# Kernel tuning notes

Measured on AMD Instinct MI355X. Metric: run time of the kernel, lower is better.

The kernel has to match this reference:

```python
import jax, jax.numpy as jnp
import numpy as np

N_NODES = 50000
N_EDGES = 1600000
LORA_R = 8


def gcn_conv(h, W, b, src, dst, n):
    # PyG GCNConv: linear transform, add self-loops, symmetric normalization,
    # scatter-add aggregation at target nodes, then bias.
    h = h @ W  # [N, out]
    ones = jnp.ones(src.shape[0], dtype=h.dtype)
    deg = jax.ops.segment_sum(ones, dst, num_segments=n) + 1.0  # +1 for self-loop
    dis = jax.lax.rsqrt(deg)  # deg >= 1 always
    norm = dis[src] * dis[dst]  # [E]
    agg = jax.ops.segment_sum(norm[:, None] * h[src], dst, num_segments=n)
    agg = agg + (dis * dis)[:, None] * h  # self-loop contribution
    return agg + b


def lora(h, A, B):
    # LoRALinear: b(a(x)) * (1/r); replaces input (not additive)
    return (h @ A) @ B * (1.0 / LORA_R)


def setup_inputs() -> dict:
    key = jax.random.key(0)
    ks = jax.random.split(key, 12)
    inp = {}
    inp['x'] = jax.random.normal(ks[0], (N_NODES, 128), dtype=jnp.float32)
    inp['edge_index'] = jax.random.randint(ks[1], (2, N_EDGES), 0, N_NODES, dtype=jnp.int64 if jax.config.jax_enable_x64 else jnp.int32)
    inp['domain_idx'] = jax.random.randint(ks[2], (N_NODES,), 0, 3, dtype=jnp.int32)
    inp['emb_table'] = jax.random.normal(ks[3], (3, 4096), dtype=jnp.float32)
    s1 = 1.0 / np.sqrt(4224.0)
    inp['W1'] = jax.random.normal(ks[4], (4224, 32), dtype=jnp.float32) * s1
    inp['b1'] = jnp.zeros((32,), dtype=jnp.float32)
    inp['A1'] = jax.random.normal(ks[5], (32, LORA_R), dtype=jnp.float32) * (1.0 / np.sqrt(32.0))
    inp['B1'] = jax.random.normal(ks[6], (LORA_R, 32), dtype=jnp.float32) * (1.0 / np.sqrt(LORA_R))
    inp['W2'] = jax.random.normal(ks[7], (32, 5), dtype=jnp.float32) * (1.0 / np.sqrt(32.0))
    inp['b2'] = jnp.zeros((5,), dtype=jnp.float32)
    inp['A2'] = jax.random.normal(ks[8], (5, LORA_R), dtype=jnp.float32) * (1.0 / np.sqrt(5.0))
    inp['B2'] = jax.random.normal(ks[9], (LORA_R, 5), dtype=jnp.float32) * (1.0 / np.sqrt(LORA_R))
    return inp


def reference(x, edge_index, domain_idx, emb_table, W1, b1, A1, B1, W2, b2, A2, B2):
    n = x.shape[0]
    src, dst = edge_index[0], edge_index[1]
    embedded = emb_table[domain_idx]  # [N, 4096]
    h = jnp.concatenate([embedded, x], axis=1)  # [N, 4224]
    h = gcn_conv(h, W1, b1, src, dst, n)
    h = lora(h, A1, B1)
    h = jax.nn.relu(h)
    h = gcn_conv(h, W2, b2, src, dst, n)
    h = lora(h, A2, B2)
    return jax.nn.log_softmax(h, axis=1)
```

## Files before the change

### kernel.cpp

```cpp
#include <hip/hip_runtime.h>
#include <hip/hip_bf16.h>
#include <hip/hip_fp16.h>


#define XDIM 128
#define ODIM 5
#define EMBDIM 4096
#define TB 8192
#define BSH 6
#define BN 64
#define ECAP2 2560

__global__ void __launch_bounds__(256) k_bin(
    const int* __restrict__ src, const int* __restrict__ dst,
    unsigned int* __restrict__ sorted, int* __restrict__ bcur, int e, int ntiles,
    const float* __restrict__ emb, const float* __restrict__ W1,
    float* __restrict__ emb_part) {
    __shared__ unsigned int staged[TB];
    __shared__ int loff[1024], rctr[1024], sbase[1024];
    int t = threadIdx.x;
    if (blockIdx.x >= ntiles) {
        int bx2 = blockIdx.x - ntiles;
        int dm = bx2 >> 5, seg = bx2 & 31;
        const float* er = emb + dm * EMBDIM + seg * 128;
        const float* wr = W1 + (size_t)seg * 128 * 32;
        int j = t & 31, kk = t >> 5;
        float acc = 0.f;
        for (int k2 = kk; k2 < 128; k2 += 8) acc += er[k2] * wr[k2 * 32 + j];
        float* p = (float*)staged;
        p[kk * 32 + j] = acc;
        __syncthreads();
        if (t < 32) {
            float s = 0.f;
            #pragma unroll
            for (int r = 0; r < 8; ++r) s += p[r * 32 + t];
            emb_part[bx2 * 32 + t] = s;
        }
        return;
    }
    int base = blockIdx.x * TB;
    int len = min(TB, e - base);
    for (int i = t; i < 1024; i += 256) { loff[i] = 0; rctr[i] = 0; }
    __syncthreads();
    for (int i = t; i < len; i += 256) atomicAdd(&loff[dst[base + i] >> BSH], 1);
    __syncthreads();
    if (t < 64) {
        int ch = t * 16;
        int v[16]; int s0 = 0;
        #pragma unroll
        for (int k = 0; k < 16; ++k) { v[k] = loff[ch + k]; s0 += v[k]; }
        int pre = s0;
        #pragma unroll
        for (int d2 = 1; d2 < 64; d2 <<= 1) {
            int up = __shfl_up(pre, d2);
            if (t >= d2) pre += up;
        }
        int excl = pre - s0;
        #pragma unroll
        for (int k = 0; k < 16; ++k) { loff[ch + k] = excl; excl += v[k]; }
    }
    __syncthreads();
    for (int i = t; i < len; i += 256) {
        int s = src[base + i], d = dst[base + i];
        int b = d >> BSH;
        int r = atomicAdd(&rctr[b], 1);
        staged[loff[b] + r] = ((unsigned int)d << 16) | (unsigned int)s;
    }
    __syncthreads();
    for (int b = t; b < 1024; b += 256) {
        int l = ((b < 1023) ? loff[b + 1] : len) - loff[b];
        if (l > 0) sbase[b] = atomicAdd(&bcur[b], l);
    }
    __syncthreads();
    for (int i = t; i < len; i += 256) {
        unsigned int u = staged[i];
        int b = (int)(u >> 22);
        int pos = sbase[b] + (i - loff[b]);
        if (pos < ECAP2) sorted[(size_t)b * ECAP2 + pos] = u;
    }
}

__global__ void __launch_bounds__(256) k_disS(
    const unsigned int* __restrict__ sorted, const int* __restrict__ bcur,
    float* __restrict__ dis, int* __restrict__ deg, int n,
    const float* __restrict__ A1, const float* __restrict__ A2,
    const float* __restrict__ B2, const float* __restrict__ b1,
    const float* __restrict__ emb_part, float* __restrict__ M2,
    float* __restrict__ b1A1, float* __restrict__ emb_proj) {
    __shared__ int h[BN];
    int t = threadIdx.x, b = blockIdx.x;
    if (t < BN) h[t] = 0;
    __syncthreads();
    int m = min(bcur[b], ECAP2);
    const unsigned int* sp = sorted + (size_t)b * ECAP2;
    for (int i = t; i < m; i += 256) {
        int d = (int)(sp[i] >> 16);
        atomicAdd(&h[d & (BN - 1)], 1);
    }
    __syncthreads();
    if (t < BN) {
        int node = (b << BSH) + t;
        if (node < n) {
            deg[node] = h[t];
            dis[node] = rsqrtf((float)(h[t] + 1));
        }
    }
    if (b == 0) {
        if (t < 25) {
            int c = t / 5, cp = t % 5;
            float s = 0.f;
            #pragma unroll
            for (int r = 0; r < 8; ++r) s += A2[c * 8 + r] * B2[r * 5 + cp];
            M2[c * 5 + cp] = s * 0.125f;
        }
        if (t >= 32 && t < 40) {
            int j = t - 32;
            float s = 0.f;
            #pragma unroll
            for (int k = 0; k < 32; ++k) s += b1[k] * A1[k * 8 + j];
            b1A1[j] = s;
        }
        if (t >= 64 && t < 160) {
            int d = (t - 64) >> 5, j = (t - 64) & 31;
            float s = 0.f;
            #pragma unroll
            for (int seg = 0; seg < 32; ++seg) s += emb_part[(d * 32 + seg) * 32 + j];
            emb_proj[d * 32 + j] = s;
        }
    }
}

__global__ void __launch_bounds__(256) k_h1(const float* __restrict__ x,
                                            const int* __restrict__ dom,
                                            const float* __restrict__ emb_proj,
                                            const float* __restrict__ W1,
                                            const float* __restrict__ A1,
                                            const float* __restrict__ dis,
                                            float* __restrict__ p1s, int n) {
    __shared__ float wb[XDIM * 32];
    __shared__ float xsT[XDIM * 68];
    __shared__ float sh1[64 * 33];
    __shared__ float sA1[256];
    __shared__ int sdom[64];
    int t = threadIdx.x;
    int row0 = blockIdx.x * 64;
    {
        const float4* w4 = (const float4*)(W1 + (size_t)EMBDIM * 32);
        float4* wb4 = (float4*)wb;
        for (int i = t; i < 1024; i += 256) wb4[i] = w4[i];
    }
    sA1[t] = A1[t];
    if (t < 64) {
        int g = row0 + t;
        sdom[t] = (g < n) ? dom[g] * 32 : 0;
    }
    for (int i = t; i < 2048; i += 256) {
        int c4 = i & 31, row = i >> 5;
        int g = row0 + row;
        float4 v = (g < n) ? ((const float4*)x)[(size_t)g * 32 + c4]
                           : make_float4(0.f, 0.f, 0.f, 0.f);
        int k0 = c4 * 4;
        xsT[(k0 + 0) * 68 + row] = v.x;
        xsT[(k0 + 1) * 68 + row] = v.y;
        xsT[(k0 + 2) * 68 + row] = v.z;
        xsT[(k0 + 3) * 68 + row] = v.w;
    }
    __syncthreads();
    int rq = t >> 4, jp = t & 15;
    float a00 = 0.f, a01 = 0.f, a10 = 0.f, a11 = 0.f;
    float a20 = 0.f, a21 = 0.f, a30 = 0.f, a31 = 0.f;
    #pragma unroll 4
    for (int k = 0; k < XDIM; ++k) {
        float4 xv = *(const float4*)(xsT + k * 68 + rq * 4);
        float2 wv = *(const float2*)(wb + k * 32 + jp * 2);
        a00 += xv.x * wv.x; a01 += xv.x * wv.y;
        a10 += xv.y * wv.x; a11 += xv.y * wv.y;
        a20 += xv.z * wv.x; a21 += xv.z * wv.y;
        a30 += xv.w * wv.x; a31 += xv.w * wv.y;
    }
    int j0 = jp * 2;
    sh1[(rq * 4 + 0) * 33 + j0]     = a00 + emb_proj[sdom[rq * 4 + 0] + j0];
    sh1[(rq * 4 + 0) * 33 + j0 + 1] = a01 + emb_proj[sdom[rq * 4 + 0] + j0 + 1];
    sh1[(rq * 4 + 1) * 33 + j0]     = a10 + emb_proj[sdom[rq * 4 + 1] + j0];
    sh1[(rq * 4 + 1) * 33 + j0 + 1] = a11 + emb_proj[sdom[rq * 4 + 1] + j0 + 1];
    sh1[(rq * 4 + 2) * 33 + j0]     = a20 + emb_proj[sdom[rq * 4 + 2] + j0];
    sh1[(rq * 4 + 2) * 33 + j0 + 1] = a21 + emb_proj[sdom[rq * 4 + 2] + j0 + 1];
    sh1[(rq * 4 + 3) * 33 + j0]     = a30 + emb_proj[sdom[rq * 4 + 3] + j0];
    sh1[(rq * 4 + 3) * 33 + j0 + 1] = a31 + emb_proj[sdom[rq * 4 + 3] + j0 + 1];
    __syncthreads();
    for (int i = t; i < 512; i += 256) {
        int row = i >> 3, jp8 = i & 7;
        int g = row0 + row;
        if (g < n) {
            float s = 0.f;
            #pragma unroll
            for (int kk = 0; kk < 32; ++kk) s += sh1[row * 33 + kk] * sA1[kk * 8 + jp8];
            p1s[(size_t)g * 8 + jp8] = dis[g] * s;
        }
    }
}

__global__ void __launch_bounds__(256) k_bagg1(
    const float* __restrict__ p1s, const unsigned int* __restrict__ sorted,
    const int* __restrict__ bcur, const int* __restrict__ deg,
    const float* __restrict__ dis, const float* __restrict__ b1A1,
    const float* __restrict__ B1, const float* __restrict__ W2,
    float* __restrict__ qs, unsigned short* __restrict__ nsrc, int n) {
    __shared__ unsigned short esrc[ECAP2];
    __shared__ int eoff[BN], sdeg[BN], rctr[BN];
    __shared__ float pacc[3][BN][8];
    __shared__ float sB1[256], sW2[160], sb[8];
    int t = threadIdx.x, b = blockIdx.x;
    int node0 = b << BSH;
    if (t < BN) rctr[t] = 0;
    sB1[t] = B1[t];
    if (t < 160) sW2[t] = W2[t];
    if (t < 8) sb[t] = b1A1[t];
    if (t < 64) {
        int node = node0 + t;
        int v = (node < n) ? deg[node] : 0;
        sdeg[t] = v;
        int pre = v;
        #pragma unroll
        for (int d2 = 1; d2 < 64; d2 <<= 1) {
            int up = __shfl_up(pre, d2);
            if (t >= d2) pre += up;
        }
        eoff[t] = pre - v;
    }
    __syncthreads();
    int m = min(bcur[b], ECAP2);
    const unsigned int* sp = sorted + (size_t)b * ECAP2;
    for (int i = t; i < m; i += 256) {
        unsigned int u = sp[i];
        int dl = (int)(u >> 16) & (BN - 1);
        int r = atomicAdd(&rctr[dl], 1);
        esrc[eoff[dl] + r] = (unsigned short)(u & 0xffffu);
    }
    __syncthreads();
    unsigned short* np = nsrc + (size_t)b * ECAP2;
    for (int i = t; i < m; i += 256) np[i] = esrc[i];
    int nodeL = t & (BN - 1), tsub = t >> BSH;
    int base0 = eoff[nodeL], c = sdeg[nodeL];
    float a[8] = {0.f, 0.f, 0.f, 0.f, 0.f, 0.f, 0.f, 0.f};
    float a2[8] = {0.f, 0.f, 0.f, 0.f, 0.f, 0.f, 0.f, 0.f};
    int k = tsub;
    for (; k + 4 < c; k += 8) {
        int s1 = esrc[base0 + k], s2 = esrc[base0 + k + 4];
        const float4* pr1 = (const float4*)(p1s + s1 * 8);
        const float4* pr2 = (const float4*)(p1s + s2 * 8);
        float4 u0 = pr1[0], u4 = pr1[1], v0 = pr2[0], v4 = pr2[1];
        a[0] += u0.x; a[1] += u0.y; a[2] += u0.z; a[3] += u0.w;
        a[4] += u4.x; a[5] += u4.y; a[6] += u4.z; a[7] += u4.w;
        a2[0] += v0.x; a2[1] += v0.y; a2[2] += v0.z; a2[3] += v0.w;
        a2[4] += v4.x; a2[5] += v4.y; a2[6] += v4.z; a2[7] += v4.w;
    }
    for (; k < c; k += 4) {
        int s1 = esrc[base0 + k];
        const float4* pr1 = (const float4*)(p1s + s1 * 8);
        float4 u0 = pr1[0], u4 = pr1[1];
        a[0] += u0.x; a[1] += u0.y; a[2] += u0.z; a[3] += u0.w;
        a[4] += u4.x; a[5] += u4.y; a[6] += u4.z; a[7] += u4.w;
    }
    #pragma unroll
    for (int j = 0; j < 8; ++j) a[j] += a2[j];
    if (tsub > 0) {
        #pragma unroll
        for (int j = 0; j < 8; ++j) pacc[tsub - 1][nodeL][j] = a[j];
    }
    __syncthreads();
    if (t < BN) {
        int node = node0 + t;
        if (node < n) {
            float dd = dis[node];
            const float4* prn = (const float4*)(p1s + node * 8);
            float4 n0 = prn[0], n4 = prn[1];
            float af[8];
            af[0] = a[0] + n0.x; af[1] = a[1] + n0.y;
            af[2] = a[2] + n0.z; af[3] = a[3] + n0.w;
            af[4] = a[4] + n4.x; af[5] = a[5] + n4.y;
            af[6] = a[6] + n4.z; af[7] = a[7] + n4.w;
            #pragma unroll
            for (int ps = 0; ps < 3; ++ps) {
                #pragma unroll
                for (int j = 0; j < 8; ++j) af[j] += pacc[ps][t][j];
            }
            #pragma unroll
            for (int j = 0; j < 8; ++j) af[j] = dd * af[j] + sb[j];
            float qv[5] = {0.f, 0.f, 0.f, 0.f, 0.f};
            #pragma unroll
            for (int c2 = 0; c2 < 32; ++c2) {
                float tv = 0.f;
                #pragma unroll
                for (int j = 0; j < 8; ++j) tv += af[j] * sB1[j * 32 + c2];
                float st = fmaxf(tv * 0.125f, 0.f);
                #pragma unroll
                for (int o = 0; o < 5; ++o) qv[o] += st * sW2[c2 * 5 + o];
            }
            #pragma unroll
            for (int o = 0; o < 5; ++o) qs[node * 8 + o] = dd * qv[o];
        }
    }
}

__global__ void __launch_bounds__(256) k_bagg2(
    const float* __restrict__ qs, const unsigned short* __restrict__ nsrc,
    const int* __restrict__ bcur, const int* __restrict__ deg,
    const float* __restrict__ dis, const float* __restrict__ b2,
    const float* __restrict__ M2, float* __restrict__ out, int n) {
    __shared__ unsigned short esrc[ECAP2];
    __shared__ int eoff[BN], sdeg[BN];
    __shared__ float pacc[3][BN][5];
    __shared__ float sM2[25], sb2[5];
    int t = threadIdx.x, b = blockIdx.x;
    int node0 = b << BSH;
    if (t < 25) sM2[t] = M2[t];
    if (t < 5) sb2[t] = b2[t];
    if (t < 64) {
        int node = node0 + t;
        int v = (node < n) ? deg[node] : 0;
        sdeg[t] = v;
        int pre = v;
        #pragma unroll
        for (int d2 = 1; d2 < 64; d2 <<= 1) {
            int up = __shfl_up(pre, d2);
            if (t >= d2) pre += up;
        }
        eoff[t] = pre - v;
    }
    __syncthreads();
    int m = min(bcur[b], ECAP2);
    const unsigned short* np = nsrc + (size_t)b * ECAP2;
    for (int i = t; i < m; i += 256) esrc[i] = np[i];
    __syncthreads();
    int nodeL = t & (BN - 1), tsub = t >> BSH;
    int base0 = eoff[nodeL], c = sdeg[nodeL];
    float a[5] = {0.f, 0.f, 0.f, 0.f, 0.f};
    float a2[5] = {0.f, 0.f, 0.f, 0.f, 0.f};
    int k = tsub;
    for (; k + 4 < c; k += 8) {
        int s1 = esrc[base0 + k], s2 = esrc[base0 + k + 4];
        const float4* q1 = (const float4*)(qs + s1 * 8);
        const float4* q2 = (const float4*)(qs + s2 * 8);
        float4 u0 = q1[0]; float u4 = qs[s1 * 8 + 4];
        float4 v0 = q2[0]; float v4 = qs[s2 * 8 + 4];
        a[0] += u0.x; a[1] += u0.y; a[2] += u0.z; a[3] += u0.w; a[4] += u4;
        a2[0] += v0.x; a2[1] += v0.y; a2[2] += v0.z; a2[3] += v0.w; a2[4] += v4;
    }
    for (; k < c; k += 4) {
        int s1 = esrc[base0 + k];
        const float4* q1 = (const float4*)(qs + s1 * 8);
        float4 u0 = q1[0]; float u4 = qs[s1 * 8 + 4];
        a[0] += u0.x; a[1] += u0.y; a[2] += u0.z; a[3] += u0.w; a[4] += u4;
    }
    #pragma unroll
    for (int j = 0; j < 5; ++j) a[j] += a2[j];
    if (tsub > 0) {
        #pragma unroll
        for (int j = 0; j < 5; ++j) pacc[tsub - 1][nodeL][j] = a[j];
    }
    __syncthreads();
    if (t < BN) {
        int node = node0 + t;
        if (node < n) {
            float dd = dis[node];
            const float4* qrn = (const float4*)(qs + node * 8);
            float4 n0 = qrn[0];
            float n4 = qs[node * 8 + 4];
            float av[5];
            av[0] = a[0] + n0.x; av[1] = a[1] + n0.y; av[2] = a[2] + n0.z;
            av[3] = a[3] + n0.w; av[4] = a[4] + n4;
            #pragma unroll
            for (int ps = 0; ps < 3; ++ps) {
                #pragma unroll
                for (int j = 0; j < 5; ++j) av[j] += pacc[ps][t][j];
            }
            #pragma unroll
            for (int j = 0; j < 5; ++j) av[j] = dd * av[j] + sb2[j];
            float z[5];
            #pragma unroll
            for (int cp = 0; cp < 5; ++cp) {
                float s = 0.f;
                #pragma unroll
                for (int c2 = 0; c2 < 5; ++c2) s += av[c2] * sM2[c2 * 5 + cp];
                z[cp] = s;
            }
            float mx = z[0];
            #pragma unroll
            for (int c2 = 1; c2 < 5; ++c2) mx = fmaxf(mx, z[c2]);
            float ssum = 0.f;
            #pragma unroll
            for (int c2 = 0; c2 < 5; ++c2) ssum += __expf(z[c2] - mx);
            float ls = __logf(ssum);
            #pragma unroll
            for (int c2 = 0; c2 < 5; ++c2) out[node * 5 + c2] = z[c2] - mx - ls;
        }
    }
}

extern "C" void kernel_launch(void* const* d_in, const int* in_sizes, int n_in,
                              void* d_out, int out_size, void* d_ws, size_t ws_size,
                              hipStream_t stream) {
    const float* x   = (const float*)d_in[0];
    const int*   ei  = (const int*)d_in[1];
    const int*   dom = (const int*)d_in[2];
    const float* emb = (const float*)d_in[3];
    const float* W1  = (const float*)d_in[4];
    const float* b1  = (const float*)d_in[5];
    const float* A1  = (const float*)d_in[6];
    const float* B1  = (const float*)d_in[7];
    const float* W2  = (const float*)d_in[8];
    const float* b2  = (const float*)d_in[9];
    const float* A2  = (const float*)d_in[10];
    const float* B2  = (const float*)d_in[11];
    float* out = (float*)d_out;

    int n = in_sizes[2];
    int e = in_sizes[1] / 2;
    const int* src = ei;
    const int* dst = ei + e;

    int ntiles = (e + TB - 1) / TB;
    int nbuck  = (n + BN - 1) >> BSH;

    char* base = (char*)d_ws;
    size_t o = 0;
    auto carve = [&](size_t bytes) {
        void* p = base + o;
        o = (o + bytes + 15) & ~(size_t)15;
        return p;
    };
    float* emb_part = (float*)carve(96 * 32 * sizeof(float));
    float* emb_proj = (float*)carve(3 * 32 * sizeof(float));
    float* M2       = (float*)carve(32 * sizeof(float));
    float* b1A1     = (float*)carve(8 * sizeof(float));
    float* dis      = (float*)carve((size_t)n * sizeof(float));
    int*   deg      = (int*)carve((size_t)n * sizeof(int));
    float* p1s      = (float*)carve((size_t)n * 8 * sizeof(float));
    float* qs       = (float*)carve((size_t)n * 8 * sizeof(float));
    int*   bcur     = (int*)carve(1024 * sizeof(int));
    unsigned int* sorted = (unsigned int*)carve((size_t)nbuck * ECAP2 * sizeof(unsigned int));
    unsigned short* nsrc = (unsigned short*)carve((size_t)nbuck * ECAP2 * sizeof(unsigned short));
    (void)ws_size; (void)n_in; (void)out_size;

    hipMemsetAsync(bcur, 0, 1024 * sizeof(int), stream);

    k_bin<<<ntiles + 96, 256, 0, stream>>>(src, dst, sorted, bcur, e, ntiles,
                                           emb, W1, emb_part);
    k_disS<<<nbuck, 256, 0, stream>>>(sorted, bcur, dis, deg, n,
                                      A1, A2, B2, b1, emb_part, M2, b1A1, emb_proj);
    k_h1<<<nbuck, 256, 0, stream>>>(x, dom, emb_proj, W1, A1, dis, p1s, n);
    k_bagg1<<<nbuck, 256, 0, stream>>>(p1s, sorted, bcur, deg, dis, b1A1, B1, W2, qs, nsrc, n);
    k_bagg2<<<nbuck, 256, 0, stream>>>(qs, nsrc, bcur, deg, dis, b2, M2, out, n);
}
```

Baseline: 177.7 us.

## Fuse degree histogram and edge bucketing into k_h1, drop k_disS kernel

Removes the separate degree/normalization kernel. Its small weight-product setup moves into the spare emb blocks of k_bin, and the per-bucket histogram, prefix scan and source-sort step move into k_h1, which now writes deg and nsrc. The aggregation kernels recompute rsqrt from degree instead of reading a dis array, and copy nsrc as 32-bit words. This removes one launch and one pass over the sorted edges, at the cost of more shared memory and work in k_h1, which may lower its occupancy.

After: 176.8 us. No clear change (-0.5%).

```diff
diff --git a/kernel.cpp b/kernel.cpp
--- a/kernel.cpp
+++ b/kernel.cpp
@@ -4,7 +4,6 @@
 
 
 #define XDIM 128
-#define ODIM 5
 #define EMBDIM 4096
 #define TB 8192
 #define BSH 6
@@ -15,7 +14,10 @@
     const int* __restrict__ src, const int* __restrict__ dst,
     unsigned int* __restrict__ sorted, int* __restrict__ bcur, int e, int ntiles,
     const float* __restrict__ emb, const float* __restrict__ W1,
-    float* __restrict__ emb_part) {
+    float* __restrict__ emb_part,
+    const float* __restrict__ A1, const float* __restrict__ A2,
+    const float* __restrict__ B2, const float* __restrict__ b1,
+    float* __restrict__ M2, float* __restrict__ b1A1) {
     __shared__ unsigned int staged[TB];
     __shared__ int loff[1024], rctr[1024], sbase[1024];
     int t = threadIdx.x;
@@ -23,7 +25,7 @@
         int bx2 = blockIdx.x - ntiles;
         int dm = bx2 >> 5, seg = bx2 & 31;
         const float* er = emb + dm * EMBDIM + seg * 128;
-        const float* wr = W1 + (size_t)seg * 128 * 32;
+        const float* wr = W1 + (size_t)(seg * 128) * 32;
         int j = t & 31, kk = t >> 5;
         float acc = 0.f;
         for (int k2 = kk; k2 < 128; k2 += 8) acc += er[k2] * wr[k2 * 32 + j];
@@ -36,6 +38,22 @@
             for (int r = 0; r < 8; ++r) s += p[r * 32 + t];
             emb_part[bx2 * 32 + t] = s;
         }
+        if (bx2 == 0) {
+            if (t < 25) {
+                int c = t / 5, cp = t % 5;
+                float s = 0.f;
+                #pragma unroll
+                for (int r = 0; r < 8; ++r) s += A2[c * 8 + r] * B2[r * 5 + cp];
+                M2[c * 5 + cp] = s * 0.125f;
+            }
+            if (t >= 32 && t < 40) {
+                int j2 = t - 32;
+                float s = 0.f;
+                #pragma unroll
+                for (int k = 0; k < 32; ++k) s += b1[k] * A1[k * 8 + j2];
+                b1A1[j2] = s;
+            }
+        }
         return;
     }
     int base = blockIdx.x * TB;
@@ -67,95 +85,59 @@
         staged[loff[b] + r] = ((unsigned int)d << 16) | (unsigned int)s;
     }
     __syncthreads();
-    for (int b = t; b < 1024; b += 256) {
-        int l = ((b < 1023) ? loff[b + 1] : len) - loff[b];
-        if (l > 0) sbase[b] = atomicAdd(&bcur[b], l);
+    for (int b2 = t; b2 < 1024; b2 += 256) {
+        int l = ((b2 < 1023) ? loff[b2 + 1] : len) - loff[b2];
+        if (l > 0) sbase[b2] = atomicAdd(&bcur[b2], l);
     }
     __syncthreads();
     for (int i = t; i < len; i += 256) {
         unsigned int u = staged[i];
-        int b = (int)(u >> 22);
-        int pos = sbase[b] + (i - loff[b]);
-        if (pos < ECAP2) sorted[(size_t)b * ECAP2 + pos] = u;
+        int b2 = (int)(u >> 22);
+        int pos = sbase[b2] + (i - loff[b2]);
+        if (pos < ECAP2) sorted[(size_t)b2 * ECAP2 + pos] = u;
     }
 }
 
-__global__ void __launch_bounds__(256) k_disS(
-    const unsigned int* __restrict__ sorted, const int* __restrict__ bcur,
-    float* __restrict__ dis, int* __restrict__ deg, int n,
-    const float* __restrict__ A1, const float* __restrict__ A2,
-    const float* __restrict__ B2, const float* __restrict__ b1,
-    const float* __restrict__ emb_part, float* __restrict__ M2,
-    float* __restrict__ b1A1, float* __restrict__ emb_proj) {
-    __shared__ int h[BN];
-    int t = threadIdx.x, b = blockIdx.x;
-    if (t < BN) h[t] = 0;
-    __syncthreads();
-    int m = min(bcur[b], ECAP2);
-    const unsigned int* sp = sorted + (size_t)b * ECAP2;
-    for (int i = t; i < m; i += 256) {
-        int d = (int)(sp[i] >> 16);
-        atomicAdd(&h[d & (BN - 1)], 1);
-    }
-    __syncthreads();
-    if (t < BN) {
-        int node = (b << BSH) + t;
-        if (node < n) {
-            deg[node] = h[t];
-            dis[node] = rsqrtf((float)(h[t] + 1));
-        }
-    }
-    if (b == 0) {
-        if (t < 25) {
-            int c = t / 5, cp = t % 5;
-            float s = 0.f;
-            #pragma unroll
-            for (int r = 0; r < 8; ++r) s += A2[c * 8 + r] * B2[r * 5 + cp];
-            M2[c * 5 + cp] = s * 0.125f;
-        }
-        if (t >= 32 && t < 40) {
-            int j = t - 32;
-            float s = 0.f;
-            #pragma unroll
-            for (int k = 0; k < 32; ++k) s += b1[k] * A1[k * 8 + j];
-            b1A1[j] = s;
-        }
-        if (t >= 64 && t < 160) {
-            int d = (t - 64) >> 5, j = (t - 64) & 31;
-            float s = 0.f;
-            #pragma unroll
-            for (int seg = 0; seg < 32; ++seg) s += emb_part[(d * 32 + seg) * 32 + j];
-            emb_proj[d * 32 + j] = s;
-        }
-    }
-}
-
-__global__ void __launch_bounds__(256) k_h1(const float* __restrict__ x,
-                                            const int* __restrict__ dom,
-                                            const float* __restrict__ emb_proj,
-                                            const float* __restrict__ W1,
-                                            const float* __restrict__ A1,
-                                            const float* __restrict__ dis,
-                                            float* __restrict__ p1s, int n) {
+__global__ void __launch_bounds__(256) k_h1(
+    const float* __restrict__ x, const int* __restrict__ dom,
+    const float* __restrict__ emb_part, const float* __restrict__ W1,
+    const float* __restrict__ A1, const unsigned int* __restrict__ sorted,
+    const int* __restrict__ bcur, float* __restrict__ p1s,
+    int* __restrict__ deg, unsigned short* __restrict__ nsrc, int n) {
     __shared__ float wb[XDIM * 32];
     __shared__ float xsT[XDIM * 68];
     __shared__ float sh1[64 * 33];
     __shared__ float sA1[256];
+    __shared__ float sproj[96];
     __shared__ int sdom[64];
-    int t = threadIdx.x;
-    int row0 = blockIdx.x * 64;
+    __shared__ int hist[64], eoff[64], rctr[64];
+    __shared__ unsigned short esrc[ECAP2];
+    int t = threadIdx.x, b = blockIdx.x;
+    int row0 = b << BSH;
+    if (t < 64) { hist[t] = 0; rctr[t] = 0; }
     {
         const float4* w4 = (const float4*)(W1 + (size_t)EMBDIM * 32);
         float4* wb4 = (float4*)wb;
         for (int i = t; i < 1024; i += 256) wb4[i] = w4[i];
-    }
-    sA1[t] = A1[t];
+        sA1[t] = A1[t];
+    }
+    if (t < 96) {
+        int d = t >> 5, j = t & 31;
+        float s = 0.f;
+        #pragma unroll
+        for (int seg = 0; seg < 32; ++seg) s += emb_part[(d * 32 + seg) * 32 + j];
+        sproj[t] = s;
+    }
     if (t < 64) {
         int g = row0 + t;
         sdom[t] = (g < n) ? dom[g] * 32 : 0;
     }
+    __syncthreads();
+    int m = min(bcur[b], ECAP2);
+    const unsigned int* sp = sorted + (size_t)b * ECAP2;
+    for (int i = t; i < m; i += 256) atomicAdd(&hist[(sp[i] >> 16) & (BN - 1)], 1);
     for (int i = t; i < 2048; i += 256) {
-        int c4 = i & 31, row = i >> 5;
+        int row = i & 63, c4 = i >> 6;
         int g = row0 + row;
         float4 v = (g < n) ? ((const float4*)x)[(size_t)g * 32 + c4]
                            : make_float4(0.f, 0.f, 0.f, 0.f);
@@ -166,6 +148,18 @@
         xsT[(k0 + 3) * 68 + row] = v.w;
     }
     __syncthreads();
+    if (t < 64) {
+        int v = hist[t];
+        int pre = v;
+        #pragma unroll
+        for (int d2 = 1; d2 < 64; d2 <<= 1) {
+            int up = __shfl_up(pre, d2);
+            if (t >= d2) pre += up;
+        }
+        eoff[t] = pre - v;
+        int g = row0 + t;
+        if (g < n) deg[g] = v;
+    }
     int rq = t >> 4, jp = t & 15;
     float a00 = 0.f, a01 = 0.f, a10 = 0.f, a11 = 0.f;
     float a20 = 0.f, a21 = 0.f, a30 = 0.f, a31 = 0.f;
@@ -179,15 +173,21 @@
         a30 += xv.w * wv.x; a31 += xv.w * wv.y;
     }
     int j0 = jp * 2;
-    sh1[(rq * 4 + 0) * 33 + j0]     = a00 + emb_proj[sdom[rq * 4 + 0] + j0];
-    sh1[(rq * 4 + 0) * 33 + j0 + 1] = a01 + emb_proj[sdom[rq * 4 + 0] + j0 + 1];
-    sh1[(rq * 4 + 1) * 33 + j0]     = a10 + emb_proj[sdom[rq * 4 + 1] + j0];
-    sh1[(rq * 4 + 1) * 33 + j0 + 1] = a11 + emb_proj[sdom[rq * 4 + 1] + j0 + 1];
-    sh1[(rq * 4 + 2) * 33 + j0]     = a20 + emb_proj[sdom[rq * 4 + 2] + j0];
-    sh1[(rq * 4 + 2) * 33 + j0 + 1] = a21 + emb_proj[sdom[rq * 4 + 2] + j0 + 1];
-    sh1[(rq * 4 + 3) * 33 + j0]     = a30 + emb_proj[sdom[rq * 4 + 3] + j0];
-    sh1[(rq * 4 + 3) * 33 + j0 + 1] = a31 + emb_proj[sdom[rq * 4 + 3] + j0 + 1];
-    __syncthreads();
+    sh1[(rq * 4 + 0) * 33 + j0]     = a00 + sproj[sdom[rq * 4 + 0] + j0];
+    sh1[(rq * 4 + 0) * 33 + j0 + 1] = a01 + sproj[sdom[rq * 4 + 0] + j0 + 1];
+    sh1[(rq * 4 + 1) * 33 + j0]     = a10 + sproj[sdom[rq * 4 + 1] + j0];
+    sh1[(rq * 4 + 1) * 33 + j0 + 1] = a11 + sproj[sdom[rq * 4 + 1] + j0 + 1];
+    sh1[(rq * 4 + 2) * 33 + j0]     = a20 + sproj[sdom[rq * 4 + 2] + j0];
+    sh1[(rq * 4 + 2) * 33 + j0 + 1] = a21 + sproj[sdom[rq * 4 + 2] + j0 + 1];
+    sh1[(rq * 4 + 3) * 33 + j0]     = a30 + sproj[sdom[rq * 4 + 3] + j0];
+    sh1[(rq * 4 + 3) * 33 + j0 + 1] = a31 + sproj[sdom[rq * 4 + 3] + j0 + 1];
+    __syncthreads();
+    for (int i = t; i < m; i += 256) {
+        unsigned int u = sp[i];
+        int dl = (int)(u >> 16) & (BN - 1);
+        int r = atomicAdd(&rctr[dl], 1);
+        esrc[eoff[dl] + r] = (unsigned short)(u & 0xffffu);
+    }
     for (int i = t; i < 512; i += 256) {
         int row = i >> 3, jp8 = i & 7;
         int g = row0 + row;
@@ -195,24 +195,30 @@
             float s = 0.f;
             #pragma unroll
             for (int kk = 0; kk < 32; ++kk) s += sh1[row * 33 + kk] * sA1[kk * 8 + jp8];
-            p1s[(size_t)g * 8 + jp8] = dis[g] * s;
-        }
+            float dd = rsqrtf((float)(hist[row] + 1));
+            p1s[(size_t)g * 8 + jp8] = dd * s;
+        }
+    }
+    __syncthreads();
+    {
+        unsigned int* npw = (unsigned int*)(nsrc + (size_t)b * ECAP2);
+        const unsigned int* ew = (const unsigned int*)esrc;
+        int mw = (m + 1) >> 1;
+        for (int i = t; i < mw; i += 256) npw[i] = ew[i];
     }
 }
 
 __global__ void __launch_bounds__(256) k_bagg1(
-    const float* __restrict__ p1s, const unsigned int* __restrict__ sorted,
+    const float* __restrict__ p1s, const unsigned short* __restrict__ nsrc,
     const int* __restrict__ bcur, const int* __restrict__ deg,
-    const float* __restrict__ dis, const float* __restrict__ b1A1,
-    const float* __restrict__ B1, const float* __restrict__ W2,
-    float* __restrict__ qs, unsigned short* __restrict__ nsrc, int n) {
+    const float* __restrict__ b1A1, const float* __restrict__ B1,
+    const float* __restrict__ W2, float* __restrict__ qs, int n) {
     __shared__ unsigned short esrc[ECAP2];
-    __shared__ int eoff[BN], sdeg[BN], rctr[BN];
+    __shared__ int eoff[BN], sdeg[BN];
     __shared__ float pacc[3][BN][8];
     __shared__ float sB1[256], sW2[160], sb[8];
     int t = threadIdx.x, b = blockIdx.x;
     int node0 = b << BSH;
-    if (t < BN) rctr[t] = 0;
     sB1[t] = B1[t];
     if (t < 160) sW2[t] = W2[t];
     if (t < 8) sb[t] = b1A1[t];
@@ -230,16 +236,13 @@
     }
     __syncthreads();
     int m = min(bcur[b], ECAP2);
-    const unsigned int* sp = sorted + (size_t)b * ECAP2;
-    for (int i = t; i < m; i += 256) {
-        unsigned int u = sp[i];
-        int dl = (int)(u >> 16) & (BN - 1);
-        int r = atomicAdd(&rctr[dl], 1);
-        esrc[eoff[dl] + r] = (unsigned short)(u & 0xffffu);
-    }
-    __syncthreads();
-    unsigned short* np = nsrc + (size_t)b * ECAP2;
-    for (int i = t; i < m; i += 256) np[i] = esrc[i];
+    {
+        const unsigned int* npw = (const unsigned int*)(nsrc + (size_t)b * ECAP2);
+        unsigned int* ew = (unsigned int*)esrc;
+        int mw = (m + 1) >> 1;
+        for (int i = t; i < mw; i += 256) ew[i] = npw[i];
+    }
+    __syncthreads();
     int nodeL = t & (BN - 1), tsub = t >> BSH;
     int base0 = eoff[nodeL], c = sdeg[nodeL];
     float a[8] = {0.f, 0.f, 0.f, 0.f, 0.f, 0.f, 0.f, 0.f};
@@ -272,7 +275,7 @@
     if (t < BN) {
         int node = node0 + t;
         if (node < n) {
-            float dd = dis[node];
+            float dd = rsqrtf((float)(sdeg[t] + 1));
             const float4* prn = (const float4*)(p1s + node * 8);
             float4 n0 = prn[0], n4 = prn[1];
             float af[8];
@@ -306,8 +309,8 @@
 __global__ void __launch_bounds__(256) k_bagg2(
     const float* __restrict__ qs, const unsigned short* __restrict__ nsrc,
     const int* __restrict__ bcur, const int* __restrict__ deg,
-    const float* __restrict__ dis, const float* __restrict__ b2,
-    const float* __restrict__ M2, float* __restrict__ out, int n) {
+    const float* __restrict__ b2, const float* __restrict__ M2,
+    float* __restrict__ out, int n) {
     __shared__ unsigned short esrc[ECAP2];
     __shared__ int eoff[BN], sdeg[BN];
     __shared__ float pacc[3][BN][5];
@@ -330,8 +333,12 @@
     }
     __syncthreads();
     int m = min(bcur[b], ECAP2);
-    const unsigned short* np = nsrc + (size_t)b * ECAP2;
-    for (int i = t; i < m; i += 256) esrc[i] = np[i];
+    {
+        const unsigned int* npw = (const unsigned int*)(nsrc + (size_t)b * ECAP2);
+        unsigned int* ew = (unsigned int*)esrc;
+        int mw = (m + 1) >> 1;
+        for (int i = t; i < mw; i += 256) ew[i] = npw[i];
+    }
     __syncthreads();
     int nodeL = t & (BN - 1), tsub = t >> BSH;
     int base0 = eoff[nodeL], c = sdeg[nodeL];
@@ -363,7 +370,7 @@
     if (t < BN) {
         int node = node0 + t;
         if (node < n) {
-            float dd = dis[node];
+            float dd = rsqrtf((float)(sdeg[t] + 1));
             const float4* qrn = (const float4*)(qs + node * 8);
             float4 n0 = qrn[0];
             float n4 = qs[node * 8 + 4];
@@ -431,10 +438,8 @@
         return p;
     };
     float* emb_part = (float*)carve(96 * 32 * sizeof(float));
-    float* emb_proj = (float*)carve(3 * 32 * sizeof(float));
     float* M2       = (float*)carve(32 * sizeof(float));
     float* b1A1     = (float*)carve(8 * sizeof(float));
-    float* dis      = (float*)carve((size_t)n * sizeof(float));
     int*   deg      = (int*)carve((size_t)n * sizeof(int));
     float* p1s      = (float*)carve((size_t)n * 8 * sizeof(float));
     float* qs       = (float*)carve((size_t)n * 8 * sizeof(float));
@@ -446,10 +451,9 @@
     hipMemsetAsync(bcur, 0, 1024 * sizeof(int), stream);
 
     k_bin<<<ntiles + 96, 256, 0, stream>>>(src, dst, sorted, bcur, e, ntiles,
-                                           emb, W1, emb_part);
-    k_disS<<<nbuck, 256, 0, stream>>>(sorted, bcur, dis, deg, n,
-                                      A1, A2, B2, b1, emb_part, M2, b1A1, emb_proj);
-    k_h1<<<nbuck, 256, 0, stream>>>(x, dom, emb_proj, W1, A1, dis, p1s, n);
-    k_bagg1<<<nbuck, 256, 0, stream>>>(p1s, sorted, bcur, deg, dis, b1A1, B1, W2, qs, nsrc, n);
-    k_bagg2<<<nbuck, 256, 0, stream>>>(qs, nsrc, bcur, deg, dis, b2, M2, out, n);
+                                           emb, W1, emb_part, A1, A2, B2, b1, M2, b1A1);
+    k_h1<<<nbuck, 256, 0, stream>>>(x, dom, emb_part, W1, A1, sorted, bcur,
+                                    p1s, deg, nsrc, n);
+    k_bagg1<<<nbuck, 256, 0, stream>>>(p1s, nsrc, bcur, deg, b1A1, B1, W2, qs, n);
+    k_bagg2<<<nbuck, 256, 0, stream>>>(qs, nsrc, bcur, deg, b2, M2, out, n);
 }
```
